# Performance work log

Hardware: AMD Instinct MI355X
Metric: run time of the kernel (lower is better)

The kernel has to match this reference:

```python
import jax, jax.numpy as jnp
import numpy as np

S = 1024; VOCAB = 100000; EMB = 300
POS_SZ = 64; CHAR_E = 50; CHAR_ENC = 128; WLEN = 16
NCHARS = 100; NPOSTAG = 50; NPOSITIONS = 1024
D = EMB + 3 * POS_SZ + CHAR_ENC  # word_rep_size = 620
BIH = 128   # per-direction LSTM hidden (bilstm_hidden_size // 2)
TLH = 256; LCC = 128; GCC = 256
NET = 8; NTAGS = 16; NREL = 16
TOKF = 2 * BIH + LCC + TLH       # 640
SENTF = 2 * TOKF + GCC           # 1536

def _p(k, shape):
    return 0.02 * jax.random.normal(k, shape, dtype=jnp.float32)

def setup_inputs():
    key = jax.random.key(0)
    ks = jax.random.split(key, 30)
    return {
        'word_inputs': jax.random.randint(ks[0], (1, S), 0, VOCAB),
        'char_inputs': jax.random.randint(ks[1], (1, S, WLEN), 0, NCHARS),
        'postag_inputs': jax.random.randint(ks[2], (1, S), 0, NPOSTAG),
        'dependency_inputs': jax.random.randint(ks[3], (1, S), 0, 64),
        'position_inputs': jax.random.randint(ks[4], (1, S), 0, NPOSITIONS),
        'topo_order': jnp.arange(S),  # children-before-parents order
        'parent': jnp.concatenate([jnp.arange(1, S), jnp.array([S])]),  # chain dep tree; root -> dummy slot S
        'pointed_token_idx': 5,
        'word_table': _p(ks[5], (VOCAB, EMB)),
        'char_table': _p(ks[6], (NCHARS, CHAR_E)),
        'char_conv_w': _p(ks[7], (CHAR_ENC, CHAR_E, 3)),
        'char_conv_b': jnp.zeros((CHAR_ENC,), jnp.float32),
        'postag_table': _p(ks[8], (NPOSTAG, POS_SZ)),
        'position_table': _p(ks[9], (NPOSITIONS, POS_SZ)),
        'lstm_f_Wx': _p(ks[10], (D, 4 * BIH)),
        'lstm_f_Wh': _p(ks[11], (BIH, 4 * BIH)),
        'lstm_f_b': jnp.zeros((4 * BIH,), jnp.float32),
        'lstm_b_Wx': _p(ks[12], (D, 4 * BIH)),
        'lstm_b_Wh': _p(ks[13], (BIH, 4 * BIH)),
        'lstm_b_b': jnp.zeros((4 * BIH,), jnp.float32),
        'word_cnn_w': _p(ks[14], (LCC, D, 3)),
        'word_cnn_b': jnp.zeros((LCC,), jnp.float32),
        'tl_Wiou': _p(ks[15], (D, 3 * TLH)),
        'tl_Uiou': _p(ks[16], (TLH, 3 * TLH)),
        'tl_biou': jnp.zeros((3 * TLH,), jnp.float32),
        'tl_Wf': _p(ks[17], (D, TLH)),
        'tl_Uf': _p(ks[18], (TLH, TLH)),
        'tl_bf': jnp.zeros((TLH,), jnp.float32),
        'sent_cnn_w': _p(ks[19], (GCC, D, 3)),
        'sent_cnn_b': jnp.zeros((GCC,), jnp.float32),
        'et_w': _p(ks[20], (GCC + TOKF, NET)),
        'et_b': jnp.zeros((NET,), jnp.float32),
        'crf_w': _p(ks[21], (SENTF, NTAGS)),
        'crf_b': jnp.zeros((NTAGS,), jnp.float32),
        'crf_trans': _p(ks[22], (NTAGS, NTAGS)),
        'rel_w': _p(ks[23], (SENTF, NREL)),
        'rel_b': jnp.zeros((NREL,), jnp.float32),
    }

def _conv1d(x, w, b):
    # x: [N, Cin, W], w: [Cout, Cin, K], padding=1 (matches nn.Conv1d(..., padding=1))
    y = jax.lax.conv_general_dilated(x, w, (1,), [(1, 1)], dimension_numbers=('NCW', 'OIW', 'NCW'))
    return y + b[None, :, None]

def _lstm(xs, Wx, Wh, b):
    H = Wh.shape[0]
    def step(carry, x):
        h, c = carry
        g = x @ Wx + h @ Wh + b
        i, f, gg, o = jnp.split(g, 4, axis=-1)
        c = jax.nn.sigmoid(f) * c + jax.nn.sigmoid(i) * jnp.tanh(gg)
        h = jax.nn.sigmoid(o) * jnp.tanh(c)
        return (h, c), h
    init = (jnp.zeros((H,), xs.dtype), jnp.zeros((H,), xs.dtype))
    _, hs = jax.lax.scan(step, init, xs)
    return hs

def _tree_lstm(x, order, parent, Wiou, Uiou, biou, Wf, Uf, bf):
    # ChildSum TreeLSTM over the whole dependency tree in topological order.
    # Equivalent to the source's per-token subtree recursion: each node's h
    # only depends on its subtree.
    Sn, H = x.shape[0], Uf.shape[0]
    xiou = x @ Wiou + biou                 # [S, 3H]
    xf = jnp.concatenate([x @ Wf + bf, jnp.zeros((1, H), x.dtype)], axis=0)  # dummy row for root's parent
    def step(carry, j):
        h, hsum, fcsum = carry
        iou = xiou[j] + hsum[j] @ Uiou
        i, o, u = jnp.split(iou, 3)
        cj = jax.nn.sigmoid(i) * jnp.tanh(u) + fcsum[j]
        hj = jax.nn.sigmoid(o) * jnp.tanh(cj)
        p = parent[j]
        f = jax.nn.sigmoid(xf[p] + hj @ Uf)  # per-child forget gate
        return (h.at[j].set(hj), hsum.at[p].add(hj), fcsum.at[p].add(f * cj)), None
    h0 = jnp.zeros((Sn, H), x.dtype)
    acc0 = jnp.zeros((Sn + 1, H), x.dtype)
    (h, _, _), _ = jax.lax.scan(step, (h0, acc0, acc0), order)
    return h

def _viterbi(emissions, trans):
    # emissions: [S, T]; trans[i, j] = score(i -> j)
    def step(score, e):
        s = score[:, None] + trans
        return jnp.max(s, axis=0) + e, jnp.argmax(s, axis=0)
    final, ptrs = jax.lax.scan(step, emissions[0], emissions[1:])
    last = jnp.argmax(final)
    def bt(tag, p):
        prev = p[tag]
        return prev, prev
    _, prevs = jax.lax.scan(bt, last, ptrs, reverse=True)
    return jnp.concatenate([prevs, last[None]])

def reference(word_inputs, char_inputs, postag_inputs, dependency_inputs, position_inputs, topo_order, parent, pointed_token_idx, word_table, char_table, char_conv_w, char_conv_b, postag_table, position_table, lstm_f_Wx, lstm_f_Wh, lstm_f_b, lstm_b_Wx, lstm_b_Wh, lstm_b_b, word_cnn_w, word_cnn_b, tl_Wiou, tl_Uiou, tl_biou, tl_Wf, tl_Uf, tl_bf, sent_cnn_w, sent_cnn_b, et_w, et_b, crf_w, crf_b, crf_trans, rel_w, rel_b):
    we = word_table[word_inputs]                                   # [1,S,EMB]
    cx = jnp.transpose(char_table[char_inputs[0]], (0, 2, 1))      # [S,CHAR_E,WLEN]
    ce = jnp.max(jax.nn.relu(_conv1d(cx, char_conv_w, char_conv_b)), axis=-1)[None]  # CharCNN -> [1,S,CHAR_ENC]
    pe = postag_table[postag_inputs]
    poe = position_table[position_inputs]
    de = position_table[dependency_inputs]                         # faithful to source bug: uses position table
    inputs = jnp.concatenate([we, ce, pe, poe, de], axis=-1)       # [1,S,D]
    x = inputs[0]
    hf = _lstm(x, lstm_f_Wx, lstm_f_Wh, lstm_f_b)
    hb = _lstm(x[::-1], lstm_b_Wx, lstm_b_Wh, lstm_b_b)[::-1]
    bilstm = jnp.concatenate([hf, hb], axis=-1)[None]              # [1,S,2*BIH]
    xc = jnp.transpose(inputs, (0, 2, 1))                          # [1,D,S]
    local_cnn = jnp.transpose(_conv1d(xc, word_cnn_w, word_cnn_b), (0, 2, 1))
    tree_h = _tree_lstm(x, topo_order, parent, tl_Wiou, tl_Uiou, tl_biou, tl_Wf, tl_Uf, tl_bf)[None]
    global_cnn = jnp.transpose(jnp.max(_conv1d(xc, sent_cnn_w, sent_cnn_b), axis=-1, keepdims=True), (0, 2, 1))  # [1,1,GCC]
    tokens_info = jnp.concatenate([bilstm, local_cnn, tree_h], axis=-1)  # [1,S,TOKF]
    ptr = tokens_info[:, pointed_token_idx, :]                     # [1,TOKF]
    ptr_info = jnp.broadcast_to(ptr[:, None, :], (1, S, TOKF))
    glob_info = jnp.broadcast_to(global_cnn, (1, S, GCC))
    sentence_encoding = jnp.concatenate([tokens_info, ptr_info, glob_info], axis=-1)  # dropout = identity (eval)
    one_vec = jnp.concatenate([global_cnn[:, 0, :], ptr], axis=-1)
    entitytype = jax.nn.softmax(one_vec @ et_w + et_b, axis=-1)
    entities = _viterbi(sentence_encoding[0] @ crf_w + crf_b, crf_trans)
    relations = jax.nn.sigmoid(sentence_encoding @ rel_w + rel_b)
    return sentence_encoding, entitytype, entities, relations
```

## Files before the change

### kernel.cpp

```cpp
#include <hip/hip_runtime.h>
#include <math.h>

#define SEQ   1024
#define DX    620
#define BIH   128
#define TLH   256
#define NTAGS 16

#define O_X      0
#define O_XGF    634880
#define O_XGB    (O_XGF + 524288)
#define O_XIOU   (O_XGB + 524288)
#define O_XF     (O_XIOU + 786432)
#define O_LCNN   (O_XF + 262400)
#define O_SCNN   (O_LCNN + 131072)
#define O_PART   (O_SCNN + 262144)
#define O_GCNN   (O_PART + 4096)
#define O_HF     (O_GCNN + 256)
#define O_HB     (O_HF + 131072)
#define O_TREEH  (O_HB + 131072)
#define O_IOUA   (O_TREEH + 262144)
#define O_FCSUM  (O_IOUA + 787200)
#define O_EMIS   (O_FCSUM + 262400)
#define O_DONE   (O_EMIS + 16384)

#define SENT 0xFFFFFFFFu

typedef float f32x4_t __attribute__((ext_vector_type(4)));

__device__ __forceinline__ float sig_f(float x){ return 1.0f/(1.0f + __expf(-x)); }
__device__ __forceinline__ float tanh_f(float x){
  float ax = fabsf(x);
  float e  = __expf(-2.0f*ax);
  float t  = (1.0f - e)/(1.0f + e);
  return x < 0.0f ? -t : t;
}
__device__ __forceinline__ int physslot(int s){ return s ^ ((s>>3)&7); }

__global__ __launch_bounds__(128) void k_embed(
    const int* __restrict__ wi, const int* __restrict__ ci,
    const int* __restrict__ postag_in, const int* __restrict__ dep_in, const int* __restrict__ pos_in,
    const float* __restrict__ word_table, const float* __restrict__ char_table,
    const float* __restrict__ ccw, const float* __restrict__ ccb,
    const float* __restrict__ postag_table, const float* __restrict__ position_table,
    float* __restrict__ x)
{
  int s = blockIdx.x;
  int tid = threadIdx.x;
  __shared__ __align__(16) float ce[50][16];
  for (int idx = tid; idx < 800; idx += 128){
    int e = idx >> 4, t = idx & 15;
    ce[e][t] = char_table[ci[s*16 + t]*50 + e];
  }
  __syncthreads();
  float* xr = x + (size_t)s*DX;
  const float* wrow = word_table + (size_t)wi[s]*300;
  for (int d = tid; d < 300; d += 128) xr[d] = wrow[d];
  {
    int oc = tid;
    const float* wp = ccw + oc*150;
    float acc[16];
    float b = ccb[oc];
    #pragma unroll
    for (int t=0;t<16;t++) acc[t] = b;
    for (int ic=0; ic<50; ic++){
      float w0 = wp[ic*3+0], w1 = wp[ic*3+1], w2 = wp[ic*3+2];
      float cv[16];
      float4 c0 = *(const float4*)&ce[ic][0];
      float4 c1 = *(const float4*)&ce[ic][4];
      float4 c2 = *(const float4*)&ce[ic][8];
      float4 c3 = *(const float4*)&ce[ic][12];
      cv[0]=c0.x;cv[1]=c0.y;cv[2]=c0.z;cv[3]=c0.w;
      cv[4]=c1.x;cv[5]=c1.y;cv[6]=c1.z;cv[7]=c1.w;
      cv[8]=c2.x;cv[9]=c2.y;cv[10]=c2.z;cv[11]=c2.w;
      cv[12]=c3.x;cv[13]=c3.y;cv[14]=c3.z;cv[15]=c3.w;
      #pragma unroll
      for (int t=0;t<16;t++){
        float a = cv[t]*w1;
        if (t > 0)  a += cv[t-1]*w0;
        if (t < 15) a += cv[t+1]*w2;
        acc[t] += a;
      }
    }
    float m = acc[0];
    #pragma unroll
    for (int t=1;t<16;t++) m = fmaxf(m, acc[t]);
    xr[300 + oc] = fmaxf(m, 0.0f);
  }
  if (tid < 64){
    int d = tid;
    xr[428 + d] = postag_table[postag_in[s]*64 + d];
    xr[492 + d] = position_table[pos_in[s]*64 + d];
    xr[556 + d] = position_table[dep_in[s]*64 + d];
  }
}

struct GemmArgs {
  const float* B[6];
  const float* bias[6];
  float*       C[6];
  int N[6]; int K[6]; int amode[6];
};

__global__ __launch_bounds__(256) void k_gemm(const float* __restrict__ x, GemmArgs ga)
{
  int z = blockIdx.z;
  int N = ga.N[z], K = ga.K[z], amode = ga.amode[z];
  int bn = blockIdx.x*64;
  if (bn >= N) return;
  int bm = blockIdx.y*64;
  const float* __restrict__ Bm = ga.B[z];
  __shared__ __align__(16) float As[20][64];
  __shared__ __align__(16) float Bs[20][64];
  int tid = threadIdx.x;
  int lane = tid & 63, kg = tid >> 6;
  int tx = tid & 15, ty = tid >> 4;
  float acc[4][4] = {{0.f}};
  for (int k0 = 0; k0 < K; k0 += 20){
    #pragma unroll
    for (int kk=0; kk<5; kk++){
      int k = kg*5 + kk;
      float av;
      if (amode == 0){
        av = x[(size_t)(bm+lane)*DX + k0 + k];
      } else {
        int kc = k0 + k;
        int d  = kc/3;
        int sh = kc - d*3 - 1;
        int row = bm + lane + sh;
        av = (row >= 0 && row < SEQ) ? x[(size_t)row*DX + d] : 0.0f;
      }
      As[k][lane] = av;
      Bs[k][lane] = (amode==0) ? Bm[(size_t)(k0+k)*N + bn + lane]
                               : Bm[(size_t)(bn+lane)*K + k0 + k];
    }
    __syncthreads();
    #pragma unroll
    for (int k=0;k<20;k++){
      float4 a = *(const float4*)&As[k][ty<<2];
      float4 b = *(const float4*)&Bs[k][tx<<2];
      acc[0][0]+=a.x*b.x; acc[0][1]+=a.x*b.y; acc[0][2]+=a.x*b.z; acc[0][3]+=a.x*b.w;
      acc[1][0]+=a.y*b.x; acc[1][1]+=a.y*b.y; acc[1][2]+=a.y*b.z; acc[1][3]+=a.y*b.w;
      acc[2][0]+=a.z*b.x; acc[2][1]+=a.z*b.y; acc[2][2]+=a.z*b.z; acc[2][3]+=a.z*b.w;
      acc[3][0]+=a.w*b.x; acc[3][1]+=a.w*b.y; acc[3][2]+=a.w*b.z; acc[3][3]+=a.w*b.w;
    }
    __syncthreads();
  }
  const float* bias = ga.bias[z];
  float* C = ga.C[z];
  float4 bb;
  bb.x = bias[bn+(tx<<2)+0]; bb.y = bias[bn+(tx<<2)+1];
  bb.z = bias[bn+(tx<<2)+2]; bb.w = bias[bn+(tx<<2)+3];
  #pragma unroll
  for (int i=0;i<4;i++){
    int row = bm + (ty<<2) + i;
    float4 o;
    o.x = acc[i][0] + bb.x; o.y = acc[i][1] + bb.y;
    o.z = acc[i][2] + bb.z; o.w = acc[i][3] + bb.w;
    *(float4*)&C[(size_t)row*N + bn + (tx<<2)] = o;
  }
}

__global__ __launch_bounds__(256) void k_gmax(const float* __restrict__ scnn, float* __restrict__ gcnn){
  int c = threadIdx.x;
  float m = -3.0e38f;
  #pragma unroll 8
  for (int s = 0; s < SEQ; s++) m = fmaxf(m, scnn[(size_t)s*256 + c]);
  gcnn[c] = m;
}

__global__ __launch_bounds__(256, 1) void k_recur(
    const float* __restrict__ xg_f, const float* __restrict__ xg_b,
    const float* __restrict__ Wh_f, const float* __restrict__ Wh_b,
    const float* __restrict__ xiou, const float* __restrict__ xf,
    const float* __restrict__ Uiou, const float* __restrict__ Uf,
    const int* __restrict__ order, const int* __restrict__ parent,
    float* __restrict__ hf, float* __restrict__ hb,
    float* tree_h, float* iou_acc, float* fcsum, unsigned* done)
{
  int bid = blockIdx.x;
  int tid = threadIdx.x;

  if (bid >= 6){
    float f0 = 1.0f + (float)tid * 1e-7f, f1 = 1.1f, f2 = 1.2f, f3 = 1.3f;
    while (__hip_atomic_load(done, __ATOMIC_RELAXED, __HIP_MEMORY_SCOPE_AGENT) < 6u){
      #pragma unroll
      for (int i=0;i<256;i++){
        f0 = fmaf(f0, 0.99999988f, 1e-9f);
        f1 = fmaf(f1, 0.99999988f, 1e-9f);
        f2 = fmaf(f2, 0.99999988f, 1e-9f);
        f3 = fmaf(f3, 0.99999988f, 1e-9f);
      }
      asm volatile("" :: "v"(f0), "v"(f1), "v"(f2), "v"(f3));
    }
    return;
  }

  if (bid >= 4){
    const float* xg  = (bid == 4) ? xg_f : xg_b;
    const float* Wh  = (bid == 4) ? Wh_f : Wh_b;
    float* hout      = (bid == 4) ? hf : hb;
    int cg = tid >> 1, rg = tid & 1;
    float4 w[4][16];
    #pragma unroll
    for (int cc=0;cc<4;cc++){
      int col = cg*4 + cc;
      #pragma unroll
      for (int r4=0;r4<16;r4++){
        int row = rg*64 + r4*4;
        w[cc][r4].x = Wh[(size_t)(row+0)*512 + col];
        w[cc][r4].y = Wh[(size_t)(row+1)*512 + col];
        w[cc][r4].z = Wh[(size_t)(row+2)*512 + col];
        w[cc][r4].w = Wh[(size_t)(row+3)*512 + col];
      }
    }
    #pragma unroll
    for (int cc=0;cc<4;cc++)
      #pragma unroll
      for (int r4=0;r4<16;r4++)
        asm volatile("" : "+v"(w[cc][r4].x), "+v"(w[cc][r4].y), "+v"(w[cc][r4].z), "+v"(w[cc][r4].w));

    __shared__ __align__(16) float lhl[BIH];
    __shared__ float lcst[BIH];
    __shared__ float gl[512];
    if (tid < BIH){ lhl[tid] = 0.f; lcst[tid] = 0.f; }
    __syncthreads();
    const float4* lhl4 = (const float4*)lhl;
    for (int st=0; st<SEQ; st++){
      int n = (bid == 4) ? st : (SEQ-1-st);
      float4 xg4 = make_float4(0.f,0.f,0.f,0.f);
      if (rg == 0) xg4 = *(const float4*)&xg[(size_t)n*512 + cg*4];
      float acc[4] = {0.f,0.f,0.f,0.f};
      #pragma unroll
      for (int r4=0;r4<16;r4++){
        float4 h4 = lhl4[rg*16 + r4];
        #pragma unroll
        for (int cc=0;cc<4;cc++)
          acc[cc] += h4.x*w[cc][r4].x + h4.y*w[cc][r4].y + h4.z*w[cc][r4].z + h4.w*w[cc][r4].w;
      }
      #pragma unroll
      for (int cc=0;cc<4;cc++) acc[cc] += __shfl_xor(acc[cc], 1);
      if (rg == 0){
        float4 o = make_float4(acc[0]+xg4.x, acc[1]+xg4.y, acc[2]+xg4.z, acc[3]+xg4.w);
        *(float4*)&gl[cg*4] = o;
      }
      __syncthreads();
      if (tid < BIH){
        float gi = gl[tid], gf = gl[BIH+tid], gg = gl[2*BIH+tid], go = gl[3*BIH+tid];
        float c = sig_f(gf)*lcst[tid] + sig_f(gi)*tanh_f(gg);
        float h = sig_f(go)*tanh_f(c);
        lcst[tid] = c;
        lhl[tid] = h;
        hout[(size_t)n*BIH + tid] = h;
      }
      __syncthreads();
    }
    if (tid == 0) __hip_atomic_fetch_add(done, 1u, __ATOMIC_RELEASE, __HIP_MEMORY_SCOPE_AGENT);
    return;
  }

  int blk = bid;
  int cg = tid >> 3, rg = tid & 7;
  int ulo = blk*64;
  float4 w[8][8];
  #pragma unroll
  for (int cc=0;cc<8;cc++){
    int c = cg*8 + cc;
    const float* Wsrc; size_t stride; int gcol;
    if (c < 192){ Wsrc = Uiou; stride = 768; gcol = (c>>6)*TLH + ulo + (c&63); }
    else        { Wsrc = Uf;   stride = 256; gcol = ulo + (c-192); }
    #pragma unroll
    for (int r4=0;r4<8;r4++){
      int row = rg*32 + r4*4;
      w[cc][r4].x = Wsrc[(size_t)(row+0)*stride + gcol];
      w[cc][r4].y = Wsrc[(size_t)(row+1)*stride + gcol];
      w[cc][r4].z = Wsrc[(size_t)(row+2)*stride + gcol];
      w[cc][r4].w = Wsrc[(size_t)(row+3)*stride + gcol];
    }
  }
  #pragma unroll
  for (int cc=0;cc<8;cc++)
    #pragma unroll
    for (int r4=0;r4<8;r4++)
      asm volatile("" : "+v"(w[cc][r4].x), "+v"(w[cc][r4].y), "+v"(w[cc][r4].z), "+v"(w[cc][r4].w));

  __shared__ __align__(16) float hl[TLH];
  __shared__ float colsum[TLH];
  __shared__ float cprev[64];
  __shared__ int ord_l[SEQ];
  __shared__ int par_l[SEQ];
  for (int i=tid; i<SEQ; i+=256){ ord_l[i] = order[i]; par_l[i] = parent[i]; }
  __syncthreads();
  const float4* hl4 = (const float4*)hl;

  for (int t=0; t<SEQ; t++){
    int n  = ord_l[t];
    int m  = (t > 0) ? ord_l[t-1] : 0;
    int pp = (t > 0) ? par_l[m] : -1;
    bool ppeq = (pp == n);

    float xi=0.f, xo=0.f, xu=0.f, ac_i=0.f, ac_o=0.f, ac_u=0.f, fcn=0.f;
    float xfv=0.f, po_i=0.f, po_o=0.f, po_u=0.f, po_f=0.f;
    if (tid < 64){
      int uu = ulo + tid;
      xi   = xiou[(size_t)n*768 + uu];
      xo   = xiou[(size_t)n*768 + 256 + uu];
      xu   = xiou[(size_t)n*768 + 512 + uu];
      ac_i = iou_acc[(size_t)n*768 + uu];
      ac_o = iou_acc[(size_t)n*768 + 256 + uu];
      ac_u = iou_acc[(size_t)n*768 + 512 + uu];
      fcn  = fcsum[(size_t)n*256 + uu];
      if (t > 0){
        xfv = xf[(size_t)pp*256 + uu];
        if (!ppeq){
          po_i = iou_acc[(size_t)pp*768 + uu];
          po_o = iou_acc[(size_t)pp*768 + 256 + uu];
          po_u = iou_acc[(size_t)pp*768 + 512 + uu];
          po_f = fcsum[(size_t)pp*256 + uu];
        }
      }
    }

    if (t > 0){
      float acc[8] = {0.f,0.f,0.f,0.f,0.f,0.f,0.f,0.f};
      int base = rg << 3;
      #pragma unroll
      for (int r4=0;r4<8;r4++){
        float4 h4 = hl4[base + (r4 ^ rg)];
        #pragma unroll
        for (int cc=0;cc<8;cc++)
          acc[cc] += h4.x*w[cc][r4].x + h4.y*w[cc][r4].y + h4.z*w[cc][r4].z + h4.w*w[cc][r4].w;
      }
      #pragma unroll
      for (int cc=0;cc<8;cc++){
        acc[cc] += __shfl_xor(acc[cc], 1);
        acc[cc] += __shfl_xor(acc[cc], 2);
        acc[cc] += __shfl_xor(acc[cc], 4);
      }
      if (rg == 0){
        *(float4*)&colsum[cg*8]     = make_float4(acc[0], acc[1], acc[2], acc[3]);
        *(float4*)&colsum[cg*8 + 4] = make_float4(acc[4], acc[5], acc[6], acc[7]);
      }
    }
    __syncthreads();

    if (tid < 64){
      int uu = ulo + tid;
      float ai = ac_i, ao = ac_o, au = ac_u, fcs = fcn;
      if (t > 0){
        float vi = colsum[tid], vo = colsum[64+tid], vuu = colsum[128+tid], vf = colsum[192+tid];
        float fg  = sig_f(xfv + vf);
        float fcc = fg * cprev[tid];
        if (ppeq){
          ai += vi; ao += vo; au += vuu; fcs += fcc;
        } else {
          iou_acc[(size_t)pp*768 + uu]       = po_i + vi;
          iou_acc[(size_t)pp*768 + 256 + uu] = po_o + vo;
          iou_acc[(size_t)pp*768 + 512 + uu] = po_u + vuu;
          fcsum[(size_t)pp*256 + uu]         = po_f + fcc;
        }
      }
      float cc = sig_f(xi + ai)*tanh_f(xu + au) + fcs;
      float hh = sig_f(xo + ao)*tanh_f(cc);
      cprev[tid] = cc;
      int s = uu >> 2;
      hl[physslot(s)*4 + (uu & 3)] = hh;
      float* tp = &tree_h[(size_t)n*TLH + uu];
      asm volatile("global_store_dword %0, %1, off sc0 sc1" :: "v"(tp), "v"(hh) : "memory");
    } else if (tid < 112){
      int p  = tid - 64;
      int qi = (p < (ulo >> 2)) ? p : p + 16;
      const float* tp = tree_h + (size_t)n*TLH + qi*4;
      union { f32x4_t v; float4 f; unsigned u[4]; } pol;
      while (true){
        asm volatile("global_load_dwordx4 %0, %1, off sc0 sc1\n\ts_waitcnt vmcnt(0)"
                     : "=v"(pol.v) : "v"(tp) : "memory");
        if ((pol.u[0] != SENT) & (pol.u[1] != SENT) & (pol.u[2] != SENT) & (pol.u[3] != SENT)) break;
      }
      *(float4*)&hl[physslot(qi)*4] = pol.f;
    }
    __syncthreads();
  }
  if (tid == 0) __hip_atomic_fetch_add(done, 1u, __ATOMIC_RELEASE, __HIP_MEMORY_SCOPE_AGENT);
}

__global__ __launch_bounds__(256) void k_assemble(
    const float* __restrict__ hf, const float* __restrict__ hb,
    const float* __restrict__ lcnn, const float* __restrict__ tree_h,
    const float* __restrict__ gcnn,
    const float* __restrict__ crf_w, const float* __restrict__ crf_b,
    const float* __restrict__ rel_w, const float* __restrict__ rel_b,
    const int* __restrict__ ptk,
    float* __restrict__ se_out, float* __restrict__ emis, float* __restrict__ rel_out)
{
  int s = blockIdx.x, tid = threadIdx.x;
  int p = ptk[0];
  __shared__ float se[1536];
  for (int d = tid; d < 1536; d += 256){
    float v;
    if      (d < 128)  v = hf[(size_t)s*128 + d];
    else if (d < 256)  v = hb[(size_t)s*128 + d-128];
    else if (d < 384)  v = lcnn[(size_t)s*128 + d-256];
    else if (d < 640)  v = tree_h[(size_t)s*256 + d-384];
    else if (d < 768)  v = hf[(size_t)p*128 + d-640];
    else if (d < 896)  v = hb[(size_t)p*128 + d-768];
    else if (d < 1024) v = lcnn[(size_t)p*128 + d-896];
    else if (d < 1280) v = tree_h[(size_t)p*256 + d-1024];
    else               v = gcnn[d-1280];
    se[d] = v;
    se_out[(size_t)s*1536 + d] = v;
  }
  __syncthreads();
  int o = tid >> 3, l = tid & 7;
  const float* W = (o < 16) ? crf_w : rel_w;
  int oc = (o < 16) ? o : (o - 16);
  float a = 0.f;
  for (int k = l; k < 1536; k += 8) a += se[k]*W[(size_t)k*16 + oc];
  for (int off = 4; off; off >>= 1) a += __shfl_down(a, off, 8);
  if (l == 0){
    if (o < 16) emis[(size_t)s*16 + o] = a + crf_b[o];
    else        rel_out[(size_t)s*16 + oc] = sig_f(a + rel_b[oc]);
  }
}

__global__ __launch_bounds__(256) void k_entity(
    const float* __restrict__ hf, const float* __restrict__ hb,
    const float* __restrict__ lcnn, const float* __restrict__ tree_h,
    const float* __restrict__ gcnn,
    const float* __restrict__ et_w, const float* __restrict__ et_b,
    const int* __restrict__ ptk, float* __restrict__ out_et)
{
  __shared__ float ov[896];
  __shared__ float lg[8];
  int tid = threadIdx.x;
  int p = ptk[0];
  for (int d = tid; d < 896; d += 256){
    float v;
    if      (d < 256) v = gcnn[d];
    else if (d < 384) v = hf[(size_t)p*128 + d-256];
    else if (d < 512) v = hb[(size_t)p*128 + d-384];
    else if (d < 640) v = lcnn[(size_t)p*128 + d-512];
    else              v = tree_h[(size_t)p*256 + d-640];
    ov[d] = v;
  }
  __syncthreads();
  int o = tid >> 5, l = tid & 31;
  float a = 0.f;
  for (int k = l; k < 896; k += 32) a += ov[k]*et_w[(size_t)k*8 + o];
  for (int off = 16; off; off >>= 1) a += __shfl_down(a, off, 32);
  if (l == 0) lg[o] = a + et_b[o];
  __syncthreads();
  if (tid == 0){
    float mx = lg[0];
    for (int i=1;i<8;i++) mx = fmaxf(mx, lg[i]);
    float e[8], sum = 0.f;
    for (int i=0;i<8;i++){ e[i] = __expf(lg[i]-mx); sum += e[i]; }
    for (int i=0;i<8;i++) out_et[i] = e[i]/sum;
  }
}

__global__ __launch_bounds__(128) void k_viterbi(
    const float* __restrict__ emis, const float* __restrict__ trans, float* __restrict__ out_e)
{
  __shared__ float ring[64][16];
  __shared__ float sc[16], nsc[16];
  __shared__ float tr[256];
  __shared__ unsigned char ptrs[1023*16];
  int tid = threadIdx.x;
  for (int i=tid; i<256; i+=128) tr[i] = trans[i];
  for (int i=tid; i<33*16; i+=128) ring[i>>4][i&15] = emis[i];
  if (tid < 16) sc[tid] = emis[tid];
  __syncthreads();
  int j = (tid & 63) >> 2, iq = tid & 3;
  for (int t=1; t<1024; t++){
    if (tid >= 64){
      int lr = tid - 64;
      int tl = t + 32;
      if (lr < 16 && tl < 1024) ring[tl & 63][lr] = emis[(size_t)tl*16 + lr];
    } else {
      float best = -3.0e38f; int barg = 0;
      #pragma unroll
      for (int ii=0; ii<4; ii++){
        int i = iq*4 + ii;
        float v = sc[i] + tr[i*16 + j];
        if (v > best){ best = v; barg = i; }
      }
      #pragma unroll
      for (int off=1; off<4; off<<=1){
        float ovv = __shfl_down(best, off, 4);
        int   oaa = __shfl_down(barg, off, 4);
        if (ovv > best){ best = ovv; barg = oaa; }
      }
      if (iq == 0){
        nsc[j] = best + ring[t & 63][j];
        ptrs[(t-1)*16 + j] = (unsigned char)barg;
      }
    }
    __syncthreads();
    if (tid < 16) sc[tid] = nsc[tid];
    __syncthreads();
  }
  if (tid == 0){
    float b = sc[0]; int last = 0;
    #pragma unroll
    for (int i=1;i<16;i++){ if (sc[i] > b){ b = sc[i]; last = i; } }
    out_e[1023] = (float)last;
    int cur = last;
    for (int t=1022; t>=0; t--){ cur = (int)ptrs[t*16 + cur]; out_e[t] = (float)cur; }
  }
}

extern "C" void kernel_launch(void* const* d_in, const int* in_sizes, int n_in,
                              void* d_out, int out_size, void* d_ws, size_t ws_size,
                              hipStream_t stream)
{
  (void)in_sizes; (void)n_in; (void)out_size; (void)ws_size;
  const int*   wi         = (const int*)d_in[0];
  const int*   ci         = (const int*)d_in[1];
  const int*   postag_in  = (const int*)d_in[2];
  const int*   dep_in     = (const int*)d_in[3];
  const int*   pos_in     = (const int*)d_in[4];
  const int*   order      = (const int*)d_in[5];
  const int*   parent     = (const int*)d_in[6];
  const int*   ptk        = (const int*)d_in[7];
  const float* word_table = (const float*)d_in[8];
  const float* char_table = (const float*)d_in[9];
  const float* ccw        = (const float*)d_in[10];
  const float* ccb        = (const float*)d_in[11];
  const float* postag_tab = (const float*)d_in[12];
  const float* pos_tab    = (const float*)d_in[13];
  const float* Wx_f       = (const float*)d_in[14];
  const float* Wh_f       = (const float*)d_in[15];
  const float* b_f        = (const float*)d_in[16];
  const float* Wx_b       = (const float*)d_in[17];
  const float* Wh_b       = (const float*)d_in[18];
  const float* b_b        = (const float*)d_in[19];
  const float* wcnn_w     = (const float*)d_in[20];
  const float* wcnn_b     = (const float*)d_in[21];
  const float* Wiou       = (const float*)d_in[22];
  const float* Uiou       = (const float*)d_in[23];
  const float* biou       = (const float*)d_in[24];
  const float* Wf_t       = (const float*)d_in[25];
  const float* Uf_t       = (const float*)d_in[26];
  const float* bf_t       = (const float*)d_in[27];
  const float* scnn_w     = (const float*)d_in[28];
  const float* scnn_b     = (const float*)d_in[29];
  const float* et_w       = (const float*)d_in[30];
  const float* et_b       = (const float*)d_in[31];
  const float* crf_w      = (const float*)d_in[32];
  const float* crf_b      = (const float*)d_in[33];
  const float* crf_trans  = (const float*)d_in[34];
  const float* rel_w      = (const float*)d_in[35];
  const float* rel_b      = (const float*)d_in[36];

  float* ws = (float*)d_ws;
  float* x      = ws + O_X;
  float* xg_f   = ws + O_XGF;
  float* xg_b   = ws + O_XGB;
  float* xiou   = ws + O_XIOU;
  float* xf     = ws + O_XF;
  float* lcnn   = ws + O_LCNN;
  float* scnn   = ws + O_SCNN;
  float* gcnn   = ws + O_GCNN;
  float* hf     = ws + O_HF;
  float* hb     = ws + O_HB;
  float* tree_h = ws + O_TREEH;
  float* iou_acc= ws + O_IOUA;
  float* fcsum  = ws + O_FCSUM;
  float* emis   = ws + O_EMIS;
  unsigned* done= (unsigned*)(ws + O_DONE);

  float* outF     = (float*)d_out;
  float* se_out   = outF;
  float* et_out   = outF + 1572864;
  float* ent_out  = outF + 1572872;
  float* rel_out  = outF + 1573896;

  hipMemsetAsync(xf, 0, (size_t)1025*256*sizeof(float), stream);
  hipMemsetAsync(iou_acc, 0, ((size_t)1025*768 + 1025*256)*sizeof(float), stream);
  hipMemsetAsync(tree_h, 0xFF, (size_t)1024*256*sizeof(float), stream);
  hipMemsetAsync(done, 0, 64, stream);

  k_embed<<<SEQ, 128, 0, stream>>>(wi, ci, postag_in, dep_in, pos_in,
                                   word_table, char_table, ccw, ccb,
                                   postag_tab, pos_tab, x);

  GemmArgs ga;
  ga.B[0]=Wx_f;  ga.bias[0]=b_f;   ga.C[0]=xg_f; ga.N[0]=512; ga.K[0]=620;  ga.amode[0]=0;
  ga.B[1]=Wx_b;  ga.bias[1]=b_b;   ga.C[1]=xg_b; ga.N[1]=512; ga.K[1]=620;  ga.amode[1]=0;
  ga.B[2]=Wiou;  ga.bias[2]=biou;  ga.C[2]=xiou; ga.N[2]=768; ga.K[2]=620;  ga.amode[2]=0;
  ga.B[3]=Wf_t;  ga.bias[3]=bf_t;  ga.C[3]=xf;   ga.N[3]=256; ga.K[3]=620;  ga.amode[3]=0;
  ga.B[4]=wcnn_w;ga.bias[4]=wcnn_b;ga.C[4]=lcnn; ga.N[4]=128; ga.K[4]=1860; ga.amode[4]=1;
  ga.B[5]=scnn_w;ga.bias[5]=scnn_b;ga.C[5]=scnn; ga.N[5]=256; ga.K[5]=1860; ga.amode[5]=1;
  k_gemm<<<dim3(12,16,6), 256, 0, stream>>>(x, ga);

  k_gmax<<<1, 256, 0, stream>>>(scnn, gcnn);

  k_recur<<<64, 256, 0, stream>>>(xg_f, xg_b, Wh_f, Wh_b, xiou, xf, Uiou, Uf_t,
                                  order, parent, hf, hb, tree_h, iou_acc, fcsum, done);

  k_assemble<<<SEQ, 256, 0, stream>>>(hf, hb, lcnn, tree_h, gcnn,
                                      crf_w, crf_b, rel_w, rel_b, ptk,
                                      se_out, emis, rel_out);

  k_entity<<<1, 256, 0, stream>>>(hf, hb, lcnn, tree_h, gcnn, et_w, et_b, ptk, et_out);

  k_viterbi<<<1, 128, 0, stream>>>(emis, crf_trans, ent_out);
}
```

Measured before the change: 3.189 ms.

## Prefetch next-step inputs in recurrences and use scoped cross-block polling

Prefetches the next timestep's input-gate values in the BiLSTM loop and the next node's xiou/xf values in the tree-LSTM loop, so the global load latency overlaps with the current step's compute. It also changes cross-block tree_h exchange: the writer issues an extra sc0-only store before the system-coherent store, and the pollers mostly use sc0 loads, with an sc0 sc1 load every fourth try. The aim is to cut per-step latency on the serial critical path. The risk is visibility and coherence behaviour across CUs from the weaker-scoped loads and the duplicate store, and the xf prefetch assumes the next step's parent index matches par_l[n].

```diff
diff --git a/kernel.cpp b/kernel.cpp
--- a/kernel.cpp
+++ b/kernel.cpp
@@ -226,10 +226,18 @@
     if (tid < BIH){ lhl[tid] = 0.f; lcst[tid] = 0.f; }
     __syncthreads();
     const float4* lhl4 = (const float4*)lhl;
+    float4 nxg4 = make_float4(0.f,0.f,0.f,0.f);
+    if (rg == 0){
+      int n0 = (bid == 4) ? 0 : (SEQ-1);
+      nxg4 = *(const float4*)&xg[(size_t)n0*512 + cg*4];
+    }
     for (int st=0; st<SEQ; st++){
       int n = (bid == 4) ? st : (SEQ-1-st);
-      float4 xg4 = make_float4(0.f,0.f,0.f,0.f);
-      if (rg == 0) xg4 = *(const float4*)&xg[(size_t)n*512 + cg*4];
+      float4 xg4 = nxg4;
+      if (rg == 0 && st+1 < SEQ){
+        int n1 = (bid == 4) ? (st+1) : (SEQ-2-st);
+        nxg4 = *(const float4*)&xg[(size_t)n1*512 + cg*4];
+      }
       float acc[4] = {0.f,0.f,0.f,0.f};
       #pragma unroll
       for (int r4=0;r4<16;r4++){
@@ -293,31 +301,42 @@
   __syncthreads();
   const float4* hl4 = (const float4*)hl;
 
+  float nxi=0.f, nxo=0.f, nxu=0.f, nxf=0.f;
+  if (tid < 64){
+    int n0 = ord_l[0];
+    int uu = ulo + tid;
+    nxi = xiou[(size_t)n0*768 + uu];
+    nxo = xiou[(size_t)n0*768 + 256 + uu];
+    nxu = xiou[(size_t)n0*768 + 512 + uu];
+  }
+
   for (int t=0; t<SEQ; t++){
     int n  = ord_l[t];
     int m  = (t > 0) ? ord_l[t-1] : 0;
     int pp = (t > 0) ? par_l[m] : -1;
     bool ppeq = (pp == n);
 
-    float xi=0.f, xo=0.f, xu=0.f, ac_i=0.f, ac_o=0.f, ac_u=0.f, fcn=0.f;
-    float xfv=0.f, po_i=0.f, po_o=0.f, po_u=0.f, po_f=0.f;
+    float xi=nxi, xo=nxo, xu=nxu, xfv=nxf;
+    float ac_i=0.f, ac_o=0.f, ac_u=0.f, fcn=0.f;
+    float po_i=0.f, po_o=0.f, po_u=0.f, po_f=0.f;
     if (tid < 64){
       int uu = ulo + tid;
-      xi   = xiou[(size_t)n*768 + uu];
-      xo   = xiou[(size_t)n*768 + 256 + uu];
-      xu   = xiou[(size_t)n*768 + 512 + uu];
+      if (t+1 < SEQ){
+        int n1 = ord_l[t+1];
+        nxi = xiou[(size_t)n1*768 + uu];
+        nxo = xiou[(size_t)n1*768 + 256 + uu];
+        nxu = xiou[(size_t)n1*768 + 512 + uu];
+        nxf = xf[(size_t)par_l[n]*256 + uu];
+      }
       ac_i = iou_acc[(size_t)n*768 + uu];
       ac_o = iou_acc[(size_t)n*768 + 256 + uu];
       ac_u = iou_acc[(size_t)n*768 + 512 + uu];
       fcn  = fcsum[(size_t)n*256 + uu];
-      if (t > 0){
-        xfv = xf[(size_t)pp*256 + uu];
-        if (!ppeq){
-          po_i = iou_acc[(size_t)pp*768 + uu];
-          po_o = iou_acc[(size_t)pp*768 + 256 + uu];
-          po_u = iou_acc[(size_t)pp*768 + 512 + uu];
-          po_f = fcsum[(size_t)pp*256 + uu];
-        }
+      if (t > 0 && !ppeq){
+        po_i = iou_acc[(size_t)pp*768 + uu];
+        po_o = iou_acc[(size_t)pp*768 + 256 + uu];
+        po_u = iou_acc[(size_t)pp*768 + 512 + uu];
+        po_f = fcsum[(size_t)pp*256 + uu];
       }
     }
 
@@ -366,15 +385,22 @@
       int s = uu >> 2;
       hl[physslot(s)*4 + (uu & 3)] = hh;
       float* tp = &tree_h[(size_t)n*TLH + uu];
+      asm volatile("global_store_dword %0, %1, off sc0"     :: "v"(tp), "v"(hh) : "memory");
       asm volatile("global_store_dword %0, %1, off sc0 sc1" :: "v"(tp), "v"(hh) : "memory");
     } else if (tid < 112){
       int p  = tid - 64;
       int qi = (p < (ulo >> 2)) ? p : p + 16;
       const float* tp = tree_h + (size_t)n*TLH + qi*4;
       union { f32x4_t v; float4 f; unsigned u[4]; } pol;
+      unsigned kk = 0;
       while (true){
-        asm volatile("global_load_dwordx4 %0, %1, off sc0 sc1\n\ts_waitcnt vmcnt(0)"
-                     : "=v"(pol.v) : "v"(tp) : "memory");
+        if ((kk & 3u) == 3u)
+          asm volatile("global_load_dwordx4 %0, %1, off sc0 sc1\n\ts_waitcnt vmcnt(0)"
+                       : "=v"(pol.v) : "v"(tp) : "memory");
+        else
+          asm volatile("global_load_dwordx4 %0, %1, off sc0\n\ts_waitcnt vmcnt(0)"
+                       : "=v"(pol.v) : "v"(tp) : "memory");
+        kk++;
         if ((pol.u[0] != SENT) & (pol.u[1] != SENT) & (pol.u[2] != SENT) & (pol.u[3] != SENT)) break;
       }
       *(float4*)&hl[physslot(qi)*4] = pol.f;
```

Result: slower. 3.450 ms (+8.2%).
